# Optimization experiments

Measured on AMD Instinct MI355X. Metric: run time of the kernel, lower is better.

Reference implementation:

```python
import jax, jax.numpy as jnp
import numpy as np

EMBED_DIM = 1024
BATCH = 256

def setup_inputs() -> dict:
    key = jax.random.key(0)
    kx, kq, kk, kv = jax.random.split(key, 4)
    D = EMBED_DIM
    x = jax.random.normal(kx, (BATCH, D), dtype=jnp.float32)
    # torch nn.Linear weights are [out, in]; y = x @ W.T
    s = 1.0 / np.sqrt(D)
    Wq = jax.random.uniform(kq, (D, D), dtype=jnp.float32, minval=-s, maxval=s)
    Wk = jax.random.uniform(kk, (D, D), dtype=jnp.float32, minval=-s, maxval=s)
    Wv = jax.random.uniform(kv, (D, D), dtype=jnp.float32, minval=-s, maxval=s)
    return {"x": x, "Wq": Wq, "Wk": Wk, "Wv": Wv}

def reference(x, Wq, Wk, Wv):
    D = x.shape[-1]
    q = x @ Wq.T  # [B, D]
    k = x @ Wk.T  # [B, D]
    v = x @ Wv.T  # [B, D]
    # rank-1 outer-product scores [B, D, D], softmax over last dim
    scores = jax.nn.softmax(q[:, :, None] * k[:, None, :] / np.sqrt(D).astype(np.float32), axis=-1)
    # scores @ v  -> [B, D]
    return jnp.einsum("bij,bj->bi", scores, v)
```

## Files before the change

kernel.cpp:

```cpp
#include <hip/hip_runtime.h>
#include <stdint.h>

#define EMBED 1024
#define BATCH 256
#define NTERM 11

#define BM 32
#define BN 64
#define BK 64
#define LPAD 72

typedef float f4 __attribute__((ext_vector_type(4)));
typedef short bf16x8 __attribute__((ext_vector_type(8)));

__device__ const float g_fact[NTERM] = {
    1.f, 1.f, 2.f, 6.f, 24.f, 120.f, 720.f, 5040.f, 40320.f, 362880.f, 3628800.f
};

__device__ __forceinline__ int packbf(float f0, float f1) {
    unsigned int u0 = __float_as_uint(f0) + 0x8000u;
    unsigned int u1 = __float_as_uint(f1) + 0x8000u;
    return (int)((u0 >> 16) | (u1 & 0xffff0000u));
}
__device__ __forceinline__ bf16x8 cvt8(f4 lo, f4 hi) {
    union { int i[4]; bf16x8 v; } u;
    u.i[0] = packbf(lo.x, lo.y);
    u.i[1] = packbf(lo.z, lo.w);
    u.i[2] = packbf(hi.x, hi.y);
    u.i[3] = packbf(hi.z, hi.w);
    return u.v;
}

__global__ __launch_bounds__(256) void gemm_qkv_mfma(
    const float* __restrict__ x,
    const float* __restrict__ Wq,
    const float* __restrict__ Wk,
    const float* __restrict__ Wv,
    float* __restrict__ qkv)
{
    const int z = blockIdx.z;
    const float* __restrict__ W = (z == 0) ? Wq : (z == 1) ? Wk : Wv;
    float* __restrict__ C = qkv + (size_t)z * BATCH * EMBED;

    const int row0 = blockIdx.x * BM;
    const int col0 = blockIdx.y * BN;
    const int tid  = threadIdx.x;

    __shared__ __align__(16) short As[BM * LPAD];
    __shared__ __align__(16) short Bs[BN * LPAD];

    const int ar = tid >> 3;
    const int ac = (tid & 7) * 8;
    const int br = tid >> 2;
    const int bc = (tid & 3) * 16;

    const float* __restrict__ ag = x + (size_t)(row0 + ar) * EMBED + ac;
    const float* __restrict__ bg = W + (size_t)(col0 + br) * EMBED + bc;

    const int lane   = tid & 63;
    const int wv     = tid >> 6;
    const int lane16 = lane & 15;
    const int quad   = lane >> 4;
    const int wrow   = (wv & 1) * 16;
    const int wcol   = (wv >> 1) * 32;

    const short* __restrict__ afp  = As + (wrow + lane16) * LPAD + quad * 8;
    const short* __restrict__ bfp0 = Bs + (wcol + lane16) * LPAD + quad * 8;
    const short* __restrict__ bfp1 = Bs + (wcol + 16 + lane16) * LPAD + quad * 8;

    f4 acc0 = {0.f, 0.f, 0.f, 0.f}, acc1 = acc0;

    f4 a0 = *(const f4*)(ag);
    f4 a1 = *(const f4*)(ag + 4);
    f4 b0 = *(const f4*)(bg);
    f4 b1 = *(const f4*)(bg + 4);
    f4 b2 = *(const f4*)(bg + 8);
    f4 b3 = *(const f4*)(bg + 12);

    for (int kt = 0; kt < EMBED; kt += BK) {
        *(bf16x8*)&As[ar * LPAD + ac]      = cvt8(a0, a1);
        *(bf16x8*)&Bs[br * LPAD + bc]      = cvt8(b0, b1);
        *(bf16x8*)&Bs[br * LPAD + bc + 8]  = cvt8(b2, b3);
        __syncthreads();

        if (kt + BK < EMBED) {
            a0 = *(const f4*)(ag + kt + BK);
            a1 = *(const f4*)(ag + kt + BK + 4);
            b0 = *(const f4*)(bg + kt + BK);
            b1 = *(const f4*)(bg + kt + BK + 4);
            b2 = *(const f4*)(bg + kt + BK + 8);
            b3 = *(const f4*)(bg + kt + BK + 12);
        }

        #pragma unroll
        for (int s = 0; s < 2; ++s) {
            bf16x8 af  = *(const bf16x8*)(afp  + s * 32);
            bf16x8 bf0 = *(const bf16x8*)(bfp0 + s * 32);
            bf16x8 bf1 = *(const bf16x8*)(bfp1 + s * 32);
            acc0 = __builtin_amdgcn_mfma_f32_16x16x32_bf16(af, bf0, acc0, 0, 0, 0);
            acc1 = __builtin_amdgcn_mfma_f32_16x16x32_bf16(af, bf1, acc1, 0, 0, 0);
        }
        __syncthreads();
    }

    const int crow = row0 + wrow + quad * 4;
    float* __restrict__ cp = C + (size_t)crow * EMBED + col0 + wcol + lane16;
    #pragma unroll
    for (int r = 0; r < 4; ++r) {
        cp[(size_t)r * EMBED +  0] = acc0[r];
        cp[(size_t)r * EMBED + 16] = acc1[r];
    }
}

__global__ __launch_bounds__(256) void attn_moments(
    const float* __restrict__ qkv,
    float* __restrict__ out)
{
    const int b   = blockIdx.x;
    const int tid = threadIdx.x;
    const float* __restrict__ Q = qkv;
    const float* __restrict__ K = qkv + (size_t)BATCH * EMBED;
    const float* __restrict__ V = qkv + (size_t)2 * BATCH * EMBED;

    f4 k4 = *(const f4*)&K[(size_t)b * EMBED + tid * 4];
    f4 v4 = *(const f4*)&V[(size_t)b * EMBED + tid * 4];

    float m1[NTERM], mv[NTERM];
    #pragma unroll
    for (int n = 0; n < NTERM; ++n) { m1[n] = 0.f; mv[n] = 0.f; }

    #pragma unroll
    for (int r = 0; r < 4; ++r) {
        float kv = k4[r], vv = v4[r];
        float p = 1.f;
        #pragma unroll
        for (int n = 0; n < NTERM; ++n) {
            m1[n] += p;
            mv[n] = __builtin_fmaf(p, vv, mv[n]);
            p *= kv;
        }
    }

    #pragma unroll
    for (int n = 0; n < NTERM; ++n) {
        #pragma unroll
        for (int off = 32; off >= 1; off >>= 1) {
            m1[n] += __shfl_xor(m1[n], off);
            mv[n] += __shfl_xor(mv[n], off);
        }
    }

    __shared__ float part[4][2 * NTERM];
    const int wave = tid >> 6;
    const int lane = tid & 63;
    if (lane == 0) {
        #pragma unroll
        for (int n = 0; n < NTERM; ++n) {
            part[wave][n]         = m1[n];
            part[wave][NTERM + n] = mv[n];
        }
    }
    __syncthreads();

    __shared__ float coef[2 * NTERM];
    if (tid < 2 * NTERM) {
        float s = part[0][tid] + part[1][tid] + part[2][tid] + part[3][tid];
        int n = (tid < NTERM) ? tid : (tid - NTERM);
        coef[tid] = s / g_fact[n];
    }
    __syncthreads();

    float c1[NTERM], cv[NTERM];
    #pragma unroll
    for (int n = 0; n < NTERM; ++n) { c1[n] = coef[n]; cv[n] = coef[NTERM + n]; }

    f4 q4 = *(const f4*)&Q[(size_t)b * EMBED + tid * 4];
    f4 res;
    #pragma unroll
    for (int r = 0; r < 4; ++r) {
        float t = q4[r] * 0.03125f;
        float den = c1[NTERM - 1];
        float num = cv[NTERM - 1];
        #pragma unroll
        for (int n = NTERM - 2; n >= 0; --n) {
            den = __builtin_fmaf(den, t, c1[n]);
            num = __builtin_fmaf(num, t, cv[n]);
        }
        res[r] = num / den;
    }

    *(f4*)&out[(size_t)b * EMBED + tid * 4] = res;
}

extern "C" void kernel_launch(void* const* d_in, const int* in_sizes, int n_in,
                              void* d_out, int out_size, void* d_ws, size_t ws_size,
                              hipStream_t stream) {
    const float* x  = (const float*)d_in[0];
    const float* Wq = (const float*)d_in[1];
    const float* Wk = (const float*)d_in[2];
    const float* Wv = (const float*)d_in[3];
    float* qkv  = (float*)d_ws;
    float* outp = (float*)d_out;

    dim3 g1(BATCH / BM, EMBED / BN, 3);
    gemm_qkv_mfma<<<g1, 256, 0, stream>>>(x, Wq, Wk, Wv, qkv);
    attn_moments<<<BATCH, 256, 0, stream>>>(qkv, outp);
}
```

Before: 83.75 us.

## Retile QKV GEMM to 32x32 tiles with BK=128 and 128-thread blocks

```diff
diff --git a/kernel.cpp b/kernel.cpp
--- a/kernel.cpp
+++ b/kernel.cpp
@@ -6,9 +6,9 @@
 #define NTERM 11
 
 #define BM 32
-#define BN 64
-#define BK 64
-#define LPAD 72
+#define BN 32
+#define BK 128
+#define LPAD (BK + 8)
 
 typedef float f4 __attribute__((ext_vector_type(4)));
 typedef short bf16x8 __attribute__((ext_vector_type(8)));
@@ -31,7 +31,7 @@
     return u.v;
 }
 
-__global__ __launch_bounds__(256) void gemm_qkv_mfma(
+__global__ __launch_bounds__(128) void gemm_qkv_mfma(
     const float* __restrict__ x,
     const float* __restrict__ Wq,
     const float* __restrict__ Wk,
@@ -49,51 +49,49 @@
     __shared__ __align__(16) short As[BM * LPAD];
     __shared__ __align__(16) short Bs[BN * LPAD];
 
-    const int ar = tid >> 3;
-    const int ac = (tid & 7) * 8;
-    const int br = tid >> 2;
-    const int bc = (tid & 3) * 16;
-
-    const float* __restrict__ ag = x + (size_t)(row0 + ar) * EMBED + ac;
-    const float* __restrict__ bg = W + (size_t)(col0 + br) * EMBED + bc;
+    const int sr = tid >> 2;
+    const int sk = (tid & 3) * 32;
+
+    const float* __restrict__ ag = x + (size_t)(row0 + sr) * EMBED + sk;
+    const float* __restrict__ bg = W + (size_t)(col0 + sr) * EMBED + sk;
 
     const int lane   = tid & 63;
     const int wv     = tid >> 6;
     const int lane16 = lane & 15;
     const int quad   = lane >> 4;
-    const int wrow   = (wv & 1) * 16;
-    const int wcol   = (wv >> 1) * 32;
+    const int wrow   = wv * 16;
 
     const short* __restrict__ afp  = As + (wrow + lane16) * LPAD + quad * 8;
-    const short* __restrict__ bfp0 = Bs + (wcol + lane16) * LPAD + quad * 8;
-    const short* __restrict__ bfp1 = Bs + (wcol + 16 + lane16) * LPAD + quad * 8;
+    const short* __restrict__ bfp0 = Bs + (lane16) * LPAD + quad * 8;
+    const short* __restrict__ bfp1 = Bs + (16 + lane16) * LPAD + quad * 8;
 
     f4 acc0 = {0.f, 0.f, 0.f, 0.f}, acc1 = acc0;
 
-    f4 a0 = *(const f4*)(ag);
-    f4 a1 = *(const f4*)(ag + 4);
-    f4 b0 = *(const f4*)(bg);
-    f4 b1 = *(const f4*)(bg + 4);
-    f4 b2 = *(const f4*)(bg + 8);
-    f4 b3 = *(const f4*)(bg + 12);
+    f4 pa[8], pb[8];
+    #pragma unroll
+    for (int i = 0; i < 8; ++i) {
+        pa[i] = *(const f4*)(ag + i * 4);
+        pb[i] = *(const f4*)(bg + i * 4);
+    }
 
     for (int kt = 0; kt < EMBED; kt += BK) {
-        *(bf16x8*)&As[ar * LPAD + ac]      = cvt8(a0, a1);
-        *(bf16x8*)&Bs[br * LPAD + bc]      = cvt8(b0, b1);
-        *(bf16x8*)&Bs[br * LPAD + bc + 8]  = cvt8(b2, b3);
+        #pragma unroll
+        for (int j = 0; j < 4; ++j) {
+            *(bf16x8*)&As[sr * LPAD + sk + 8 * j] = cvt8(pa[2 * j], pa[2 * j + 1]);
+            *(bf16x8*)&Bs[sr * LPAD + sk + 8 * j] = cvt8(pb[2 * j], pb[2 * j + 1]);
+        }
         __syncthreads();
 
         if (kt + BK < EMBED) {
-            a0 = *(const f4*)(ag + kt + BK);
-            a1 = *(const f4*)(ag + kt + BK + 4);
-            b0 = *(const f4*)(bg + kt + BK);
-            b1 = *(const f4*)(bg + kt + BK + 4);
-            b2 = *(const f4*)(bg + kt + BK + 8);
-            b3 = *(const f4*)(bg + kt + BK + 12);
-        }
-
-        #pragma unroll
-        for (int s = 0; s < 2; ++s) {
+            #pragma unroll
+            for (int i = 0; i < 8; ++i) {
+                pa[i] = *(const f4*)(ag + kt + BK + i * 4);
+                pb[i] = *(const f4*)(bg + kt + BK + i * 4);
+            }
+        }
+
+        #pragma unroll
+        for (int s = 0; s < 4; ++s) {
             bf16x8 af  = *(const bf16x8*)(afp  + s * 32);
             bf16x8 bf0 = *(const bf16x8*)(bfp0 + s * 32);
             bf16x8 bf1 = *(const bf16x8*)(bfp1 + s * 32);
@@ -104,7 +102,7 @@
     }
 
     const int crow = row0 + wrow + quad * 4;
-    float* __restrict__ cp = C + (size_t)crow * EMBED + col0 + wcol + lane16;
+    float* __restrict__ cp = C + (size_t)crow * EMBED + col0 + lane16;
     #pragma unroll
     for (int r = 0; r < 4; ++r) {
         cp[(size_t)r * EMBED +  0] = acc0[r];
@@ -203,6 +201,6 @@
     float* outp = (float*)d_out;
 
     dim3 g1(BATCH / BM, EMBED / BN, 3);
-    gemm_qkv_mfma<<<g1, 256, 0, stream>>>(x, Wq, Wk, Wv, qkv);
+    gemm_qkv_mfma<<<g1, 128, 0, stream>>>(x, Wq, Wk, Wv, qkv);
     attn_moments<<<BATCH, 256, 0, stream>>>(qkv, outp);
 }
```

After: 95.34 us. 13.8% more time.
